# Kernel tuning notes

Hardware: AMD Instinct MI355X
Metric: run time of the kernel (lower is better)

The kernel has to match this reference:

```python
import jax, jax.numpy as jnp
import numpy as np

SEQ, BATCH, HID, NLAYERS = 2048, 16, 1024, 2


def setup_inputs() -> dict:
    key = jax.random.key(0)
    ks = jax.random.split(key, 3)
    scale = 1.0 / np.sqrt(HID)
    x = jax.random.normal(ks[0], (SEQ, BATCH, HID), dtype=jnp.float32)
    W0 = jax.random.normal(ks[1], (HID, 3 * HID), dtype=jnp.float32) * scale
    b0 = jnp.zeros((2 * HID,), dtype=jnp.float32)
    W1 = jax.random.normal(ks[2], (HID, 3 * HID), dtype=jnp.float32) * scale
    b1 = jnp.zeros((2 * HID,), dtype=jnp.float32)
    return {"x": x, "W0": W0, "b0": b0, "W1": W1, "b1": b1}


def _sru_layer(x, W, b):
    # x: [L, B, H]; W: [H, 3H]; b: [2H]
    L, B, H = x.shape
    U = jnp.einsum('lbd,dk->lbk', x, W)  # [L, B, 3H]
    x_tilde = U[..., :H]
    bf, br = b[:H], b[H:]
    f = jax.nn.sigmoid(U[..., H:2 * H] + bf)  # forget gate [L,B,H]
    r = jax.nn.sigmoid(U[..., 2 * H:] + br)   # reset gate  [L,B,H]

    def step(c_prev, inp):
        xt_t, f_t = inp
        c_t = f_t * c_prev + (1.0 - f_t) * xt_t
        return c_t, c_t

    c0 = jnp.zeros((B, H), dtype=x.dtype)
    _, cs = jax.lax.scan(step, c0, (x_tilde, f))  # cs: [L, B, H]
    h = r * cs + (1.0 - r) * x  # highway connection
    return h


def reference(x, W0, b0, W1, b1):
    h = _sru_layer(x, W0, b0)
    h = _sru_layer(h, W1, b1)
    return h[-1:]  # [1, B, H], matching `out[-1:]`
```

## Files before the change

kernel.cpp:

```cpp
#include <hip/hip_runtime.h>

#define SEQ    2048
#define BATCH  16
#define HID    1024
#define M_TOT  (SEQ*BATCH)
#define NCH    (BATCH*HID)
#define NCHUNK 64
#define TCHUNK (SEQ/NCHUNK)
#define NSEG   128

typedef __attribute__((ext_vector_type(8))) short          short8;
typedef __attribute__((ext_vector_type(8))) unsigned short ushort8_t;
typedef __attribute__((ext_vector_type(4))) float          floatx4;

__device__ __forceinline__ unsigned short f32_to_bf16(float f) {
  unsigned int u = __float_as_uint(f);
  u += 0x7FFFu + ((u >> 16) & 1u);
  return (unsigned short)(u >> 16);
}
__device__ __forceinline__ float bf16_to_f32(unsigned short h) {
  return __uint_as_float(((unsigned int)h) << 16);
}
__device__ __forceinline__ float sigmoidf_(float x) {
  return 1.f / (1.f + __expf(-x));
}


__device__ __forceinline__ void cast_swizzle_body(const float* __restrict__ src,
    unsigned short* __restrict__ dst, int mt, int kt, int t) {
  __shared__ unsigned short tile[4096];
  const int r = t >> 1, kh = (t & 1) * 16;
  const float* sp = src + (size_t)(mt * 128 + r) * 1024 + kt * 32 + kh;
  float4 v0 = *(const float4*)(sp + 0);
  float4 v1 = *(const float4*)(sp + 4);
  float4 v2 = *(const float4*)(sp + 8);
  float4 v3 = *(const float4*)(sp + 12);
  ushort8_t u0, u1;
  u0[0]=f32_to_bf16(v0.x); u0[1]=f32_to_bf16(v0.y); u0[2]=f32_to_bf16(v0.z); u0[3]=f32_to_bf16(v0.w);
  u0[4]=f32_to_bf16(v1.x); u0[5]=f32_to_bf16(v1.y); u0[6]=f32_to_bf16(v1.z); u0[7]=f32_to_bf16(v1.w);
  u1[0]=f32_to_bf16(v2.x); u1[1]=f32_to_bf16(v2.y); u1[2]=f32_to_bf16(v2.z); u1[3]=f32_to_bf16(v2.w);
  u1[4]=f32_to_bf16(v3.x); u1[5]=f32_to_bf16(v3.y); u1[6]=f32_to_bf16(v3.z); u1[7]=f32_to_bf16(v3.w);
  const int c = r >> 4, lr = r & 15, q0 = kh >> 3;
  const int unit0 = c * 64 + (q0 << 4) + lr;
  *(ushort8_t*)&tile[unit0 * 8]        = u0;
  *(ushort8_t*)&tile[(unit0 + 16) * 8] = u1;
  __syncthreads();
  const size_t base = ((size_t)mt * 32 + kt) * 4096;
  *(ushort8_t*)&dst[base + t * 16]     = *(const ushort8_t*)&tile[t * 16];
  *(ushort8_t*)&dst[base + t * 16 + 8] = *(const ushort8_t*)&tile[t * 16 + 8];
}

__device__ __forceinline__ void w_prep_body(const float* __restrict__ W,
    unsigned short* __restrict__ Wsw, int nt, int kt, int t) {
  __shared__ unsigned short tile[4096];
  const int kk = t >> 3, n0 = (t & 7) * 16;
  const float* sp = W + (size_t)(kt * 32 + kk) * 3072 + nt * 128 + n0;
  float v[16];
#pragma unroll
  for (int i = 0; i < 16; i += 4) {
    float4 f = *(const float4*)(sp + i);
    v[i] = f.x; v[i+1] = f.y; v[i+2] = f.z; v[i+3] = f.w;
  }
  const int cbase = (n0 >> 4) * 64 + ((kk >> 3) << 4);
#pragma unroll
  for (int j = 0; j < 16; j++)
    tile[(cbase + j) * 8 + (kk & 7)] = f32_to_bf16(v[j]);
  __syncthreads();
  const size_t base = ((size_t)nt * 32 + kt) * 4096;
  *(ushort8_t*)&Wsw[base + t * 16]     = *(const ushort8_t*)&tile[t * 16];
  *(ushort8_t*)&Wsw[base + t * 16 + 8] = *(const ushort8_t*)&tile[t * 16 + 8];
}

__global__ __launch_bounds__(256) void prep_all(const float* __restrict__ x,
    const float* __restrict__ W0, const float* __restrict__ W1,
    unsigned short* __restrict__ xsw, unsigned short* __restrict__ W0sw,
    unsigned short* __restrict__ W1sw) {
  const int id = blockIdx.x, t = threadIdx.x;
  if (id < 8192)        cast_swizzle_body(x, xsw, id >> 5, id & 31, t);
  else if (id < 8960)   w_prep_body(W0, W0sw, (id - 8192) >> 5, (id - 8192) & 31, t);
  else                  w_prep_body(W1, W1sw, (id - 8960) >> 5, (id - 8960) & 31, t);
}

typedef __attribute__((address_space(1))) const unsigned int GUI;
typedef __attribute__((address_space(3))) unsigned int LUI;
__device__ __forceinline__ void gl16(const unsigned short* g, unsigned short* l) {
  __builtin_amdgcn_global_load_lds((GUI*)g, (LUI*)l, 16, 0, 0);
}
__device__ __forceinline__ void barrier_fence() {
  asm volatile("s_barrier" ::: "memory");
}

__global__ __launch_bounds__(512, 2) void gemm_pipe(
    const unsigned short* __restrict__ A, const unsigned short* __restrict__ B,
    unsigned short* __restrict__ Xt, unsigned short* __restrict__ Fo,
    unsigned short* __restrict__ Ro, const float* __restrict__ bias)
{
  __shared__ unsigned short lds[65536];
  const int tid = threadIdx.x;
  const int wave = tid >> 6, lane = tid & 63;
  const int wm = wave >> 2, wn = wave & 3;
  const int id = blockIdx.x;
  const int xcd = id & 7, slot = id >> 3;
  const int g = slot / 96, r = slot % 96;
  const int bn = r >> 3;
  const int bm = xcd * 16 + g * 8 + (r & 7);

  const unsigned short* aSrc0 = A + ((size_t)(2 * bm + 0) * 32) * 4096 + tid * 8;
  const unsigned short* aSrc1 = A + ((size_t)(2 * bm + 1) * 32) * 4096 + tid * 8;
  const unsigned short* bSrc0 = B + ((size_t)(2 * bn + 0) * 32) * 4096 + tid * 8;
  const unsigned short* bSrc1 = B + ((size_t)(2 * bn + 1) * 32) * 4096 + tid * 8;

  floatx4 acc[8][4];
#pragma unroll
  for (int i = 0; i < 8; i++)
#pragma unroll
    for (int j = 0; j < 4; j++)
#pragma unroll
      for (int rr = 0; rr < 4; rr++) acc[i][j][rr] = 0.f;

#pragma unroll
  for (int u = 0; u < 3; ++u) {
    unsigned short* d = &lds[u * 16384 + wave * 512];
    gl16(aSrc0 + (size_t)u * 4096, d);
    gl16(aSrc1 + (size_t)u * 4096, d + 4096);
    gl16(bSrc0 + (size_t)u * 4096, d + 8192);
    gl16(bSrc1 + (size_t)u * 4096, d + 12288);
  }
  asm volatile("s_waitcnt vmcnt(0)" ::: "memory");
  barrier_fence();

  const int aoff = wm * 4096 + lane * 8;
  const int boff = 8192 + (wn >> 1) * 4096 + (wn & 1) * 2048 + lane * 8;

#pragma unroll 1
  for (int t = 0; t < 32; ++t) {
    const int sb = (t & 3) * 16384;
    const int u = t + 3;
    const unsigned short* As = &lds[sb + aoff];
    const unsigned short* Bs = &lds[sb + boff];
    short8 br[4], ar[4];
#pragma unroll
    for (int nj = 0; nj < 4; ++nj) br[nj] = *(const short8*)(Bs + nj * 512);
#pragma unroll
    for (int mi = 0; mi < 4; ++mi) ar[mi] = *(const short8*)(As + mi * 512);
    if (u < 32) {
      unsigned short* d = &lds[(u & 3) * 16384 + wave * 512];
      gl16(aSrc0 + (size_t)u * 4096, d);
      gl16(aSrc1 + (size_t)u * 4096, d + 4096);
    }
    __builtin_amdgcn_s_setprio(1);
#pragma unroll
    for (int mi = 0; mi < 4; ++mi)
#pragma unroll
      for (int nj = 0; nj < 4; ++nj)
        acc[mi][nj] = __builtin_amdgcn_mfma_f32_16x16x32_bf16(ar[mi], br[nj], acc[mi][nj], 0, 0, 0);
    __builtin_amdgcn_s_setprio(0);
#pragma unroll
    for (int mi = 0; mi < 4; ++mi) ar[mi] = *(const short8*)(As + (4 + mi) * 512);
    if (u < 32) {
      unsigned short* d = &lds[(u & 3) * 16384 + wave * 512];
      gl16(bSrc0 + (size_t)u * 4096, d + 8192);
      gl16(bSrc1 + (size_t)u * 4096, d + 12288);
    }
    __builtin_amdgcn_s_setprio(1);
#pragma unroll
    for (int mi = 0; mi < 4; ++mi)
#pragma unroll
      for (int nj = 0; nj < 4; ++nj)
        acc[4 + mi][nj] = __builtin_amdgcn_mfma_f32_16x16x32_bf16(ar[mi], br[nj], acc[4 + mi][nj], 0, 0, 0);
    __builtin_amdgcn_s_setprio(0);
    if (t <= 28)      asm volatile("s_waitcnt vmcnt(8)" ::: "memory");
    else if (t == 29) asm volatile("s_waitcnt vmcnt(4)" ::: "memory");
    else if (t == 30) asm volatile("s_waitcnt vmcnt(0)" ::: "memory");
    barrier_fence();
  }

  const int region = bn >> 2;
  const int cc = lane & 15, q = lane >> 4;
  const int lc0 = (bn & 3) * 256 + wn * 64 + cc;
  const int row0 = bm * 256 + wm * 128 + q * 4;
  if (region == 0) {
#pragma unroll
    for (int mi = 0; mi < 8; ++mi)
#pragma unroll
      for (int rg = 0; rg < 4; ++rg)
#pragma unroll
        for (int nj = 0; nj < 4; ++nj)
          Xt[(size_t)(row0 + mi * 16 + rg) * 1024 + lc0 + nj * 16] =
              f32_to_bf16(acc[mi][nj][rg]);
  } else {
    unsigned short* O = (region == 1) ? Fo : Ro;
    const float* bp = bias + (region - 1) * 1024;
    float bb[4];
#pragma unroll
    for (int nj = 0; nj < 4; ++nj) bb[nj] = bp[lc0 + nj * 16];
#pragma unroll
    for (int mi = 0; mi < 8; ++mi)
#pragma unroll
      for (int rg = 0; rg < 4; ++rg)
#pragma unroll
        for (int nj = 0; nj < 4; ++nj) {
          float s = sigmoidf_(acc[mi][nj][rg] + bb[nj]);
          O[(size_t)(row0 + mi * 16 + rg) * 1024 + lc0 + nj * 16] = f32_to_bf16(s);
        }
  }
}

__global__ __launch_bounds__(512, 2) void gemm2_scan(
    const unsigned short* __restrict__ A, const unsigned short* __restrict__ B,
    const float* __restrict__ bias, float* __restrict__ Pseg, float* __restrict__ Sseg)
{
  __shared__ unsigned short lds[65536];
  const int tid = threadIdx.x;
  const int wave = tid >> 6, lane = tid & 63;
  const int wm = wave >> 2, wn = wave & 3;
  const int id = blockIdx.x;
  const int xcd = id & 7, slot = id >> 3;
  const int bn = slot >> 4;
  const int bm = xcd * 16 + (slot & 15);

  const unsigned short* aSrc0 = A + ((size_t)(2 * bm + 0) * 32) * 4096 + tid * 8;
  const unsigned short* aSrc1 = A + ((size_t)(2 * bm + 1) * 32) * 4096 + tid * 8;
  const unsigned short* bxSrc = B + ((size_t)bn * 32) * 4096 + tid * 8;
  const unsigned short* bfSrc = B + ((size_t)(8 + bn) * 32) * 4096 + tid * 8;

  floatx4 ax[8][2], af[8][2];
#pragma unroll
  for (int i = 0; i < 8; i++)
#pragma unroll
    for (int j = 0; j < 2; j++)
#pragma unroll
      for (int rr = 0; rr < 4; rr++) { ax[i][j][rr] = 0.f; af[i][j][rr] = 0.f; }

#pragma unroll
  for (int u = 0; u < 3; ++u) {
    unsigned short* d = &lds[u * 16384 + wave * 512];
    gl16(aSrc0 + (size_t)u * 4096, d);
    gl16(aSrc1 + (size_t)u * 4096, d + 4096);
    gl16(bxSrc + (size_t)u * 4096, d + 8192);
    gl16(bfSrc + (size_t)u * 4096, d + 12288);
  }
  asm volatile("s_waitcnt vmcnt(0)" ::: "memory");
  barrier_fence();

  const int aoff  = wm * 4096 + lane * 8;
  const int bxoff = 8192  + wn * 1024 + lane * 8;
  const int bfoff = 12288 + wn * 1024 + lane * 8;

#pragma unroll 1
  for (int t = 0; t < 32; ++t) {
    const int sb = (t & 3) * 16384;
    const int u = t + 3;
    const unsigned short* As  = &lds[sb + aoff];
    const unsigned short* Bxs = &lds[sb + bxoff];
    const unsigned short* Bfs = &lds[sb + bfoff];
    short8 bx[2], bf[2], ar[4];
#pragma unroll
    for (int nj = 0; nj < 2; ++nj) {
      bx[nj] = *(const short8*)(Bxs + nj * 512);
      bf[nj] = *(const short8*)(Bfs + nj * 512);
    }
#pragma unroll
    for (int mi = 0; mi < 4; ++mi) ar[mi] = *(const short8*)(As + mi * 512);
    if (u < 32) {
      unsigned short* d = &lds[(u & 3) * 16384 + wave * 512];
      gl16(aSrc0 + (size_t)u * 4096, d);
      gl16(aSrc1 + (size_t)u * 4096, d + 4096);
    }
    __builtin_amdgcn_s_setprio(1);
#pragma unroll
    for (int mi = 0; mi < 4; ++mi)
#pragma unroll
      for (int nj = 0; nj < 2; ++nj) {
        ax[mi][nj] = __builtin_amdgcn_mfma_f32_16x16x32_bf16(ar[mi], bx[nj], ax[mi][nj], 0, 0, 0);
        af[mi][nj] = __builtin_amdgcn_mfma_f32_16x16x32_bf16(ar[mi], bf[nj], af[mi][nj], 0, 0, 0);
      }
    __builtin_amdgcn_s_setprio(0);
#pragma unroll
    for (int mi = 0; mi < 4; ++mi) ar[mi] = *(const short8*)(As + (4 + mi) * 512);
    if (u < 32) {
      unsigned short* d = &lds[(u & 3) * 16384 + wave * 512];
      gl16(bxSrc + (size_t)u * 4096, d + 8192);
      gl16(bfSrc + (size_t)u * 4096, d + 12288);
    }
    __builtin_amdgcn_s_setprio(1);
#pragma unroll
    for (int mi = 0; mi < 4; ++mi)
#pragma unroll
      for (int nj = 0; nj < 2; ++nj) {
        ax[4 + mi][nj] = __builtin_amdgcn_mfma_f32_16x16x32_bf16(ar[mi], bx[nj], ax[4 + mi][nj], 0, 0, 0);
        af[4 + mi][nj] = __builtin_amdgcn_mfma_f32_16x16x32_bf16(ar[mi], bf[nj], af[4 + mi][nj], 0, 0, 0);
      }
    __builtin_amdgcn_s_setprio(0);
    if (t <= 28)      asm volatile("s_waitcnt vmcnt(8)" ::: "memory");
    else if (t == 29) asm volatile("s_waitcnt vmcnt(4)" ::: "memory");
    else if (t == 30) asm volatile("s_waitcnt vmcnt(0)" ::: "memory");
    barrier_fence();
  }

  const int q = lane >> 4, cc = lane & 15;
  float pv[2][4], sv[2][4];
#pragma unroll
  for (int nj = 0; nj < 2; ++nj) {
    float bb = bias[bn * 128 + wn * 32 + nj * 16 + cc];
#pragma unroll
    for (int rg = 0; rg < 4; ++rg) {
      float p = 1.f, s = 0.f;
#pragma unroll
      for (int mi = 0; mi < 8; ++mi) {
        float f  = sigmoidf_(af[mi][nj][rg] + bb);
        float xt = ax[mi][nj][rg];
        s = f * s + (1.f - f) * xt;
        p *= f;
      }
      pv[nj][rg] = p; sv[nj][rg] = s;
    }
  }
  float* lf = (float*)lds;
  __syncthreads();
  if (wm == 0) {
#pragma unroll
    for (int nj = 0; nj < 2; ++nj)
#pragma unroll
      for (int rg = 0; rg < 4; ++rg) {
        const int idx = (((wn * 64 + lane) * 4 + rg) * 2 + nj) * 2;
        lf[idx]     = pv[nj][rg];
        lf[idx + 1] = sv[nj][rg];
      }
  }
  __syncthreads();
  if (wm == 1) {
#pragma unroll
    for (int nj = 0; nj < 2; ++nj) {
      const int h = bn * 128 + wn * 32 + nj * 16 + cc;
#pragma unroll
      for (int rg = 0; rg < 4; ++rg) {
        const int idx = (((wn * 64 + lane) * 4 + rg) * 2 + nj) * 2;
        float plo = lf[idx], slo = lf[idx + 1];
        float phi = pv[nj][rg], shi = sv[nj][rg];
        const size_t off = (size_t)bm * NCH + (q * 4 + rg) * 1024 + h;
        Pseg[off] = plo * phi;
        Sseg[off] = phi * slo + shi;
      }
    }
  }
}

__global__ __launch_bounds__(256) void scan_pass1(
    const unsigned short* __restrict__ Xt, const unsigned short* __restrict__ F,
    float* __restrict__ P, float* __restrict__ S) {
  const int ch = (blockIdx.x * 256 + threadIdx.x) * 8;
  const int chunk = blockIdx.y;
  size_t idx = (size_t)chunk * TCHUNK * NCH + ch;
  float p[8], s[8];
#pragma unroll
  for (int j = 0; j < 8; j++) { p[j] = 1.f; s[j] = 0.f; }
  for (int t = 0; t < TCHUNK; ++t) {
    ushort8_t fv = *(const ushort8_t*)&F[idx];
    ushort8_t xv = *(const ushort8_t*)&Xt[idx];
#pragma unroll
    for (int j = 0; j < 8; j++) {
      float f  = bf16_to_f32(fv[j]);
      float xt = bf16_to_f32(xv[j]);
      s[j] = f * s[j] + (1.f - f) * xt;
      p[j] *= f;
    }
    idx += NCH;
  }
  float4* P4 = (float4*)&P[(size_t)chunk * NCH + ch];
  float4* S4 = (float4*)&S[(size_t)chunk * NCH + ch];
  P4[0] = make_float4(p[0], p[1], p[2], p[3]);
  P4[1] = make_float4(p[4], p[5], p[6], p[7]);
  S4[0] = make_float4(s[0], s[1], s[2], s[3]);
  S4[1] = make_float4(s[4], s[5], s[6], s[7]);
}

__global__ __launch_bounds__(256) void combine_c0(
    const float* __restrict__ P, const float* __restrict__ S, float* __restrict__ C0) {
  const int ch = blockIdx.x * 256 + threadIdx.x;
  float c = 0.f;
#pragma unroll 4
  for (int k = 0; k < NCHUNK; ++k) {
    C0[(size_t)k * NCH + ch] = c;
    c = P[(size_t)k * NCH + ch] * c + S[(size_t)k * NCH + ch];
  }
}

#define TPAD 4112
__global__ __launch_bounds__(256) void scan1_pass2_fused(
    const unsigned short* __restrict__ Xt, const unsigned short* __restrict__ F,
    const unsigned short* __restrict__ R, unsigned short* __restrict__ xsw,
    const float* __restrict__ C0, unsigned short* __restrict__ h1last)
{
  __shared__ unsigned short st[4 * TPAD];
  const int hb = blockIdx.x;
  const int chunk = blockIdx.y;
  const int tid = threadIdx.x;
  const int b = tid >> 4, hg = tid & 15;
  const int h0 = hb * 128 + hg * 8;
  const int ch = b * 1024 + h0;
  const int tl   = hg >> 2;
  const int usub = (hg & 3) * 16 + b;

  float c[8];
  {
    const float4* C4 = (const float4*)&C0[(size_t)chunk * NCH + ch];
    float4 a = C4[0], d = C4[1];
    c[0]=a.x; c[1]=a.y; c[2]=a.z; c[3]=a.w; c[4]=d.x; c[5]=d.y; c[6]=d.z; c[7]=d.w;
  }

  size_t idx = (size_t)chunk * TCHUNK * NCH + ch;
  for (int t8 = 0; t8 < TCHUNK / 8; ++t8) {
#pragma unroll
    for (int ts = 0; ts < 8; ++ts) {
      const int t = chunk * TCHUNK + t8 * 8 + ts;
      ushort8_t fv = *(const ushort8_t*)&F[idx];
      ushort8_t xv = *(const ushort8_t*)&Xt[idx];
      ushort8_t rv = *(const ushort8_t*)&R[idx];
      const size_t soff = ((size_t)(t >> 3) * 32 + (h0 >> 5)) * 4096
                        + (size_t)(((t & 7) * 64 + usub) * 8);
      ushort8_t xo = *(const ushort8_t*)&xsw[soff];
      ushort8_t hv;
#pragma unroll
      for (int j = 0; j < 8; ++j) {
        float f  = bf16_to_f32(fv[j]);
        float xt = bf16_to_f32(xv[j]);
        c[j] = f * c[j] + (1.f - f) * xt;
        float r  = bf16_to_f32(rv[j]);
        float xval = bf16_to_f32(xo[j]);
        hv[j] = f32_to_bf16(r * c[j] + (1.f - r) * xval);
      }
      *(ushort8_t*)&st[tl * TPAD + (ts * 64 + usub) * 8] = hv;
      if (t == SEQ - 1) *(ushort8_t*)&h1last[ch] = hv;
      idx += NCH;
    }
    __syncthreads();
    const size_t gbase = (((size_t)chunk * (TCHUNK / 8) + t8) * 32 + hb * 4) * 4096;
#pragma unroll
    for (int tl2 = 0; tl2 < 4; ++tl2) {
      size_t gdst = gbase + (size_t)tl2 * 4096 + tid * 16;
      *(ushort8_t*)&xsw[gdst]     = *(const ushort8_t*)&st[tl2 * TPAD + tid * 16];
      *(ushort8_t*)&xsw[gdst + 8] = *(const ushort8_t*)&st[tl2 * TPAD + tid * 16 + 8];
    }
    __syncthreads();
  }
}

__global__ __launch_bounds__(256) void r2_kernel(
    const unsigned short* __restrict__ h1last, const float* __restrict__ W1,
    const float* __restrict__ b1, float* __restrict__ r2) {
  __shared__ float xrow[1024];
  const int b = blockIdx.x, nq = blockIdx.y, tid = threadIdx.x;
  for (int i = tid; i < 1024; i += 256)
    xrow[i] = bf16_to_f32(h1last[b * 1024 + i]);
  __syncthreads();
  const int n = nq * 256 + tid;
  float acc = b1[1024 + n];
  for (int d = 0; d < 1024; ++d)
    acc += xrow[d] * W1[(size_t)d * 3072 + 2048 + n];
  r2[b * 1024 + n] = sigmoidf_(acc);
}

__global__ __launch_bounds__(256) void final_l2(
    const float* __restrict__ Pseg, const float* __restrict__ Sseg,
    const float* __restrict__ r2, const unsigned short* __restrict__ h1last,
    float* __restrict__ out) {
  const int ch = blockIdx.x * 256 + threadIdx.x;
  float c = 0.f;
#pragma unroll 8
  for (int k = 0; k < NSEG; ++k)
    c = Pseg[(size_t)k * NCH + ch] * c + Sseg[(size_t)k * NCH + ch];
  float r = r2[ch];
  float x = bf16_to_f32(h1last[ch]);
  out[ch] = r * c + (1.f - r) * x;
}

extern "C" void kernel_launch(void* const* d_in, const int* in_sizes, int n_in,
                              void* d_out, int out_size, void* d_ws, size_t ws_size,
                              hipStream_t stream) {
  const float* x  = (const float*)d_in[0];
  const float* W0 = (const float*)d_in[1];
  const float* b0 = (const float*)d_in[2];
  const float* W1 = (const float*)d_in[3];
  const float* b1 = (const float*)d_in[4];
  float* out = (float*)d_out;

  char* ws = (char*)d_ws;
  auto alloc = [&](size_t bytes) {
    char* p = ws; ws += (bytes + 255) & ~(size_t)255; return p;
  };
  const size_t NE = (size_t)M_TOT * HID;
  unsigned short* xsw   = (unsigned short*)alloc(NE * 2);
  unsigned short* W0sw  = (unsigned short*)alloc((size_t)3072 * 1024 * 2);
  unsigned short* W1sw  = (unsigned short*)alloc((size_t)3072 * 1024 * 2);
  unsigned short* Xt    = (unsigned short*)alloc(NE * 2);
  unsigned short* F     = (unsigned short*)alloc(NE * 2);
  unsigned short* R     = (unsigned short*)alloc(NE * 2);
  unsigned short* h1last= (unsigned short*)alloc((size_t)NCH * 2);
  float* P    = (float*)alloc((size_t)NCHUNK * NCH * 4);
  float* S    = (float*)alloc((size_t)NCHUNK * NCH * 4);
  float* C0   = (float*)alloc((size_t)NCHUNK * NCH * 4);
  float* Pseg = (float*)alloc((size_t)NSEG * NCH * 4);
  float* Sseg = (float*)alloc((size_t)NSEG * NCH * 4);
  float* r2   = (float*)alloc((size_t)NCH * 4);

  dim3 blk256(256);
  prep_all<<<dim3(9728), blk256, 0, stream>>>(x, W0, W1, xsw, W0sw, W1sw);
  gemm_pipe<<<dim3(1536), dim3(512), 0, stream>>>(xsw, W0sw, Xt, F, R, b0);
  scan_pass1<<<dim3(8, NCHUNK), blk256, 0, stream>>>(Xt, F, P, S);
  combine_c0<<<dim3(NCH / 256), blk256, 0, stream>>>(P, S, C0);
  scan1_pass2_fused<<<dim3(8, NCHUNK), blk256, 0, stream>>>(Xt, F, R, xsw, C0, h1last);
  r2_kernel<<<dim3(16, 4), blk256, 0, stream>>>(h1last, W1, b1, r2);
  gemm2_scan<<<dim3(1024), dim3(512), 0, stream>>>(xsw, W1sw, b1, Pseg, Sseg);
  final_l2<<<dim3(NCH / 256), blk256, 0, stream>>>(Pseg, Sseg, r2, h1last, out);
}
```

Baseline: 731.6 us.

## Fuse layer-1 scan pass1 into GEMM epilogue with 8-step segments

Layer-1 GEMM now tiles so each block computes matching x~, f and r columns for 128 rows, which is 8 timesteps of 16 batch. The epilogue computes per-segment scan products and sums directly from the accumulators and writes Pseg1/Sseg1, so the separate scan_pass1 kernel and its re-read of Xt/F are gone. The scan pass2 now runs over 256 segments of 8 steps, and combine_c0 walks 256 segments instead of 64. In exchange the GEMM tile shape changes to 128x(3x128), which uses a smaller per-operand tile and may cost GEMM efficiency, and the P/S/C0 buffers grow.

```diff
diff --git a/kernel.cpp b/kernel.cpp
--- a/kernel.cpp
+++ b/kernel.cpp
@@ -5,8 +5,7 @@
 #define HID    1024
 #define M_TOT  (SEQ*BATCH)
 #define NCH    (BATCH*HID)
-#define NCHUNK 64
-#define TCHUNK (SEQ/NCHUNK)
+#define NSEG1  256
 #define NSEG   128
 
 typedef __attribute__((ext_vector_type(8))) short          short8;
@@ -90,10 +89,11 @@
   asm volatile("s_barrier" ::: "memory");
 }
 
-__global__ __launch_bounds__(512, 2) void gemm_pipe(
+__global__ __launch_bounds__(512, 2) void gemm1_scan(
     const unsigned short* __restrict__ A, const unsigned short* __restrict__ B,
     unsigned short* __restrict__ Xt, unsigned short* __restrict__ Fo,
-    unsigned short* __restrict__ Ro, const float* __restrict__ bias)
+    unsigned short* __restrict__ Ro, const float* __restrict__ bias,
+    float* __restrict__ Pseg1, float* __restrict__ Sseg1)
 {
   __shared__ unsigned short lds[65536];
   const int tid = threadIdx.x;
@@ -101,73 +101,81 @@
   const int wm = wave >> 2, wn = wave & 3;
   const int id = blockIdx.x;
   const int xcd = id & 7, slot = id >> 3;
-  const int g = slot / 96, r = slot % 96;
-  const int bn = r >> 3;
-  const int bm = xcd * 16 + g * 8 + (r & 7);
-
-  const unsigned short* aSrc0 = A + ((size_t)(2 * bm + 0) * 32) * 4096 + tid * 8;
-  const unsigned short* aSrc1 = A + ((size_t)(2 * bm + 1) * 32) * 4096 + tid * 8;
-  const unsigned short* bSrc0 = B + ((size_t)(2 * bn + 0) * 32) * 4096 + tid * 8;
-  const unsigned short* bSrc1 = B + ((size_t)(2 * bn + 1) * 32) * 4096 + tid * 8;
-
-  floatx4 acc[8][4];
-#pragma unroll
-  for (int i = 0; i < 8; i++)
-#pragma unroll
-    for (int j = 0; j < 4; j++)
-#pragma unroll
-      for (int rr = 0; rr < 4; rr++) acc[i][j][rr] = 0.f;
+  const int bn = slot >> 5;
+  const int bm = xcd * 32 + (slot & 31);
+
+  const unsigned short* aSrc  = A + ((size_t)bm * 32) * 4096 + tid * 8;
+  const unsigned short* bxSrc = B + ((size_t)bn * 32) * 4096 + tid * 8;
+  const unsigned short* bfSrc = B + ((size_t)(8 + bn) * 32) * 4096 + tid * 8;
+  const unsigned short* brSrc = B + ((size_t)(16 + bn) * 32) * 4096 + tid * 8;
+
+  floatx4 ax[4][2], af[4][2], arr[4][2];
+#pragma unroll
+  for (int i = 0; i < 4; i++)
+#pragma unroll
+    for (int j = 0; j < 2; j++)
+#pragma unroll
+      for (int rr = 0; rr < 4; rr++) { ax[i][j][rr] = 0.f; af[i][j][rr] = 0.f; arr[i][j][rr] = 0.f; }
 
 #pragma unroll
   for (int u = 0; u < 3; ++u) {
     unsigned short* d = &lds[u * 16384 + wave * 512];
-    gl16(aSrc0 + (size_t)u * 4096, d);
-    gl16(aSrc1 + (size_t)u * 4096, d + 4096);
-    gl16(bSrc0 + (size_t)u * 4096, d + 8192);
-    gl16(bSrc1 + (size_t)u * 4096, d + 12288);
+    gl16(aSrc  + (size_t)u * 4096, d);
+    gl16(bxSrc + (size_t)u * 4096, d + 4096);
+    gl16(bfSrc + (size_t)u * 4096, d + 8192);
+    gl16(brSrc + (size_t)u * 4096, d + 12288);
   }
   asm volatile("s_waitcnt vmcnt(0)" ::: "memory");
   barrier_fence();
 
-  const int aoff = wm * 4096 + lane * 8;
-  const int boff = 8192 + (wn >> 1) * 4096 + (wn & 1) * 2048 + lane * 8;
+  const int aoff = wm * 2048 + lane * 8;
+  const int bxo  = 4096  + wn * 1024 + lane * 8;
+  const int bfo  = 8192  + wn * 1024 + lane * 8;
+  const int bro  = 12288 + wn * 1024 + lane * 8;
 
 #pragma unroll 1
   for (int t = 0; t < 32; ++t) {
     const int sb = (t & 3) * 16384;
     const int u = t + 3;
-    const unsigned short* As = &lds[sb + aoff];
-    const unsigned short* Bs = &lds[sb + boff];
-    short8 br[4], ar[4];
-#pragma unroll
-    for (int nj = 0; nj < 4; ++nj) br[nj] = *(const short8*)(Bs + nj * 512);
+    const unsigned short* As  = &lds[sb + aoff];
+    const unsigned short* Bxs = &lds[sb + bxo];
+    const unsigned short* Bfs = &lds[sb + bfo];
+    const unsigned short* Brs = &lds[sb + bro];
+    short8 ar[4], bx[2], bf[2], br2[2];
+#pragma unroll
+    for (int nj = 0; nj < 2; ++nj) {
+      bx[nj] = *(const short8*)(Bxs + nj * 512);
+      bf[nj] = *(const short8*)(Bfs + nj * 512);
+    }
 #pragma unroll
     for (int mi = 0; mi < 4; ++mi) ar[mi] = *(const short8*)(As + mi * 512);
     if (u < 32) {
       unsigned short* d = &lds[(u & 3) * 16384 + wave * 512];
-      gl16(aSrc0 + (size_t)u * 4096, d);
-      gl16(aSrc1 + (size_t)u * 4096, d + 4096);
+      gl16(aSrc  + (size_t)u * 4096, d);
+      gl16(bxSrc + (size_t)u * 4096, d + 4096);
     }
     __builtin_amdgcn_s_setprio(1);
 #pragma unroll
     for (int mi = 0; mi < 4; ++mi)
 #pragma unroll
-      for (int nj = 0; nj < 4; ++nj)
-        acc[mi][nj] = __builtin_amdgcn_mfma_f32_16x16x32_bf16(ar[mi], br[nj], acc[mi][nj], 0, 0, 0);
+      for (int nj = 0; nj < 2; ++nj) {
+        ax[mi][nj] = __builtin_amdgcn_mfma_f32_16x16x32_bf16(ar[mi], bx[nj], ax[mi][nj], 0, 0, 0);
+        af[mi][nj] = __builtin_amdgcn_mfma_f32_16x16x32_bf16(ar[mi], bf[nj], af[mi][nj], 0, 0, 0);
+      }
     __builtin_amdgcn_s_setprio(0);
 #pragma unroll
-    for (int mi = 0; mi < 4; ++mi) ar[mi] = *(const short8*)(As + (4 + mi) * 512);
+    for (int nj = 0; nj < 2; ++nj) br2[nj] = *(const short8*)(Brs + nj * 512);
     if (u < 32) {
       unsigned short* d = &lds[(u & 3) * 16384 + wave * 512];
-      gl16(bSrc0 + (size_t)u * 4096, d + 8192);
-      gl16(bSrc1 + (size_t)u * 4096, d + 12288);
+      gl16(bfSrc + (size_t)u * 4096, d + 8192);
+      gl16(brSrc + (size_t)u * 4096, d + 12288);
     }
     __builtin_amdgcn_s_setprio(1);
 #pragma unroll
     for (int mi = 0; mi < 4; ++mi)
 #pragma unroll
-      for (int nj = 0; nj < 4; ++nj)
-        acc[4 + mi][nj] = __builtin_amdgcn_mfma_f32_16x16x32_bf16(ar[mi], br[nj], acc[4 + mi][nj], 0, 0, 0);
+      for (int nj = 0; nj < 2; ++nj)
+        arr[mi][nj] = __builtin_amdgcn_mfma_f32_16x16x32_bf16(ar[mi], br2[nj], arr[mi][nj], 0, 0, 0);
     __builtin_amdgcn_s_setprio(0);
     if (t <= 28)      asm volatile("s_waitcnt vmcnt(8)" ::: "memory");
     else if (t == 29) asm volatile("s_waitcnt vmcnt(4)" ::: "memory");
@@ -175,34 +183,60 @@
     barrier_fence();
   }
 
-  const int region = bn >> 2;
-  const int cc = lane & 15, q = lane >> 4;
-  const int lc0 = (bn & 3) * 256 + wn * 64 + cc;
-  const int row0 = bm * 256 + wm * 128 + q * 4;
-  if (region == 0) {
-#pragma unroll
-    for (int mi = 0; mi < 8; ++mi)
-#pragma unroll
-      for (int rg = 0; rg < 4; ++rg)
-#pragma unroll
-        for (int nj = 0; nj < 4; ++nj)
-          Xt[(size_t)(row0 + mi * 16 + rg) * 1024 + lc0 + nj * 16] =
-              f32_to_bf16(acc[mi][nj][rg]);
-  } else {
-    unsigned short* O = (region == 1) ? Fo : Ro;
-    const float* bp = bias + (region - 1) * 1024;
-    float bb[4];
-#pragma unroll
-    for (int nj = 0; nj < 4; ++nj) bb[nj] = bp[lc0 + nj * 16];
-#pragma unroll
-    for (int mi = 0; mi < 8; ++mi)
-#pragma unroll
-      for (int rg = 0; rg < 4; ++rg)
-#pragma unroll
-        for (int nj = 0; nj < 4; ++nj) {
-          float s = sigmoidf_(acc[mi][nj][rg] + bb[nj]);
-          O[(size_t)(row0 + mi * 16 + rg) * 1024 + lc0 + nj * 16] = f32_to_bf16(s);
-        }
+  const int q = lane >> 4, cc = lane & 15;
+  const int h0 = bn * 128 + wn * 32 + cc;
+  const int row0 = bm * 128 + wm * 64 + q * 4;
+  float bbf[2], bbr[2];
+#pragma unroll
+  for (int nj = 0; nj < 2; ++nj) {
+    bbf[nj] = bias[h0 + nj * 16];
+    bbr[nj] = bias[1024 + h0 + nj * 16];
+  }
+  float pv[2][4], sv[2][4];
+#pragma unroll
+  for (int nj = 0; nj < 2; ++nj)
+#pragma unroll
+    for (int rg = 0; rg < 4; ++rg) {
+      float p = 1.f, s = 0.f;
+#pragma unroll
+      for (int mi = 0; mi < 4; ++mi) {
+        float xt = ax[mi][nj][rg];
+        float f  = sigmoidf_(af[mi][nj][rg] + bbf[nj]);
+        float rr = sigmoidf_(arr[mi][nj][rg] + bbr[nj]);
+        const size_t ro = (size_t)(row0 + mi * 16 + rg) * 1024 + h0 + nj * 16;
+        Xt[ro] = f32_to_bf16(xt);
+        Fo[ro] = f32_to_bf16(f);
+        Ro[ro] = f32_to_bf16(rr);
+        s = f * s + (1.f - f) * xt;
+        p *= f;
+      }
+      pv[nj][rg] = p; sv[nj][rg] = s;
+    }
+  float* lf = (float*)lds;
+  __syncthreads();
+  if (wm == 0) {
+#pragma unroll
+    for (int nj = 0; nj < 2; ++nj)
+#pragma unroll
+      for (int rg = 0; rg < 4; ++rg) {
+        const int idx = (((wn * 64 + lane) * 4 + rg) * 2 + nj) * 2;
+        lf[idx]     = pv[nj][rg];
+        lf[idx + 1] = sv[nj][rg];
+      }
+  }
+  __syncthreads();
+  if (wm == 1) {
+#pragma unroll
+    for (int nj = 0; nj < 2; ++nj)
+#pragma unroll
+      for (int rg = 0; rg < 4; ++rg) {
+        const int idx = (((wn * 64 + lane) * 4 + rg) * 2 + nj) * 2;
+        float plo = lf[idx], slo = lf[idx + 1];
+        float phi = pv[nj][rg], shi = sv[nj][rg];
+        const size_t off = (size_t)bm * NCH + (q * 4 + rg) * 1024 + h0 + nj * 16;
+        Pseg1[off] = plo * phi;
+        Sseg1[off] = phi * slo + shi;
+      }
   }
 }
 
@@ -346,41 +380,12 @@
   }
 }
 
-__global__ __launch_bounds__(256) void scan_pass1(
-    const unsigned short* __restrict__ Xt, const unsigned short* __restrict__ F,
-    float* __restrict__ P, float* __restrict__ S) {
-  const int ch = (blockIdx.x * 256 + threadIdx.x) * 8;
-  const int chunk = blockIdx.y;
-  size_t idx = (size_t)chunk * TCHUNK * NCH + ch;
-  float p[8], s[8];
-#pragma unroll
-  for (int j = 0; j < 8; j++) { p[j] = 1.f; s[j] = 0.f; }
-  for (int t = 0; t < TCHUNK; ++t) {
-    ushort8_t fv = *(const ushort8_t*)&F[idx];
-    ushort8_t xv = *(const ushort8_t*)&Xt[idx];
-#pragma unroll
-    for (int j = 0; j < 8; j++) {
-      float f  = bf16_to_f32(fv[j]);
-      float xt = bf16_to_f32(xv[j]);
-      s[j] = f * s[j] + (1.f - f) * xt;
-      p[j] *= f;
-    }
-    idx += NCH;
-  }
-  float4* P4 = (float4*)&P[(size_t)chunk * NCH + ch];
-  float4* S4 = (float4*)&S[(size_t)chunk * NCH + ch];
-  P4[0] = make_float4(p[0], p[1], p[2], p[3]);
-  P4[1] = make_float4(p[4], p[5], p[6], p[7]);
-  S4[0] = make_float4(s[0], s[1], s[2], s[3]);
-  S4[1] = make_float4(s[4], s[5], s[6], s[7]);
-}
-
 __global__ __launch_bounds__(256) void combine_c0(
     const float* __restrict__ P, const float* __restrict__ S, float* __restrict__ C0) {
   const int ch = blockIdx.x * 256 + threadIdx.x;
   float c = 0.f;
-#pragma unroll 4
-  for (int k = 0; k < NCHUNK; ++k) {
+#pragma unroll 8
+  for (int k = 0; k < NSEG1; ++k) {
     C0[(size_t)k * NCH + ch] = c;
     c = P[(size_t)k * NCH + ch] * c + S[(size_t)k * NCH + ch];
   }
@@ -409,40 +414,37 @@
     c[0]=a.x; c[1]=a.y; c[2]=a.z; c[3]=a.w; c[4]=d.x; c[5]=d.y; c[6]=d.z; c[7]=d.w;
   }
 
-  size_t idx = (size_t)chunk * TCHUNK * NCH + ch;
-  for (int t8 = 0; t8 < TCHUNK / 8; ++t8) {
-#pragma unroll
-    for (int ts = 0; ts < 8; ++ts) {
-      const int t = chunk * TCHUNK + t8 * 8 + ts;
-      ushort8_t fv = *(const ushort8_t*)&F[idx];
-      ushort8_t xv = *(const ushort8_t*)&Xt[idx];
-      ushort8_t rv = *(const ushort8_t*)&R[idx];
-      const size_t soff = ((size_t)(t >> 3) * 32 + (h0 >> 5)) * 4096
-                        + (size_t)(((t & 7) * 64 + usub) * 8);
-      ushort8_t xo = *(const ushort8_t*)&xsw[soff];
-      ushort8_t hv;
-#pragma unroll
-      for (int j = 0; j < 8; ++j) {
-        float f  = bf16_to_f32(fv[j]);
-        float xt = bf16_to_f32(xv[j]);
-        c[j] = f * c[j] + (1.f - f) * xt;
-        float r  = bf16_to_f32(rv[j]);
-        float xval = bf16_to_f32(xo[j]);
-        hv[j] = f32_to_bf16(r * c[j] + (1.f - r) * xval);
-      }
-      *(ushort8_t*)&st[tl * TPAD + (ts * 64 + usub) * 8] = hv;
-      if (t == SEQ - 1) *(ushort8_t*)&h1last[ch] = hv;
-      idx += NCH;
-    }
-    __syncthreads();
-    const size_t gbase = (((size_t)chunk * (TCHUNK / 8) + t8) * 32 + hb * 4) * 4096;
-#pragma unroll
-    for (int tl2 = 0; tl2 < 4; ++tl2) {
-      size_t gdst = gbase + (size_t)tl2 * 4096 + tid * 16;
-      *(ushort8_t*)&xsw[gdst]     = *(const ushort8_t*)&st[tl2 * TPAD + tid * 16];
-      *(ushort8_t*)&xsw[gdst + 8] = *(const ushort8_t*)&st[tl2 * TPAD + tid * 16 + 8];
-    }
-    __syncthreads();
+  size_t idx = (size_t)chunk * 8 * NCH + ch;
+#pragma unroll
+  for (int ts = 0; ts < 8; ++ts) {
+    const int t = chunk * 8 + ts;
+    ushort8_t fv = *(const ushort8_t*)&F[idx];
+    ushort8_t xv = *(const ushort8_t*)&Xt[idx];
+    ushort8_t rv = *(const ushort8_t*)&R[idx];
+    const size_t soff = ((size_t)(t >> 3) * 32 + (h0 >> 5)) * 4096
+                      + (size_t)(((t & 7) * 64 + usub) * 8);
+    ushort8_t xo = *(const ushort8_t*)&xsw[soff];
+    ushort8_t hv;
+#pragma unroll
+    for (int j = 0; j < 8; ++j) {
+      float f  = bf16_to_f32(fv[j]);
+      float xt = bf16_to_f32(xv[j]);
+      c[j] = f * c[j] + (1.f - f) * xt;
+      float r  = bf16_to_f32(rv[j]);
+      float xval = bf16_to_f32(xo[j]);
+      hv[j] = f32_to_bf16(r * c[j] + (1.f - r) * xval);
+    }
+    *(ushort8_t*)&st[tl * TPAD + (ts * 64 + usub) * 8] = hv;
+    if (t == SEQ - 1) *(ushort8_t*)&h1last[ch] = hv;
+    idx += NCH;
+  }
+  __syncthreads();
+  const size_t gbase = ((size_t)chunk * 32 + hb * 4) * 4096;
+#pragma unroll
+  for (int tl2 = 0; tl2 < 4; ++tl2) {
+    size_t gdst = gbase + (size_t)tl2 * 4096 + tid * 16;
+    *(ushort8_t*)&xsw[gdst]     = *(const ushort8_t*)&st[tl2 * TPAD + tid * 16];
+    *(ushort8_t*)&xsw[gdst + 8] = *(const ushort8_t*)&st[tl2 * TPAD + tid * 16 + 8];
   }
 }
 
@@ -497,19 +499,18 @@
   unsigned short* F     = (unsigned short*)alloc(NE * 2);
   unsigned short* R     = (unsigned short*)alloc(NE * 2);
   unsigned short* h1last= (unsigned short*)alloc((size_t)NCH * 2);
-  float* P    = (float*)alloc((size_t)NCHUNK * NCH * 4);
-  float* S    = (float*)alloc((size_t)NCHUNK * NCH * 4);
-  float* C0   = (float*)alloc((size_t)NCHUNK * NCH * 4);
-  float* Pseg = (float*)alloc((size_t)NSEG * NCH * 4);
-  float* Sseg = (float*)alloc((size_t)NSEG * NCH * 4);
-  float* r2   = (float*)alloc((size_t)NCH * 4);
+  float* Pseg1 = (float*)alloc((size_t)NSEG1 * NCH * 4);
+  float* Sseg1 = (float*)alloc((size_t)NSEG1 * NCH * 4);
+  float* C0    = (float*)alloc((size_t)NSEG1 * NCH * 4);
+  float* Pseg  = (float*)alloc((size_t)NSEG * NCH * 4);
+  float* Sseg  = (float*)alloc((size_t)NSEG * NCH * 4);
+  float* r2    = (float*)alloc((size_t)NCH * 4);
 
   dim3 blk256(256);
   prep_all<<<dim3(9728), blk256, 0, stream>>>(x, W0, W1, xsw, W0sw, W1sw);
-  gemm_pipe<<<dim3(1536), dim3(512), 0, stream>>>(xsw, W0sw, Xt, F, R, b0);
-  scan_pass1<<<dim3(8, NCHUNK), blk256, 0, stream>>>(Xt, F, P, S);
-  combine_c0<<<dim3(NCH / 256), blk256, 0, stream>>>(P, S, C0);
-  scan1_pass2_fused<<<dim3(8, NCHUNK), blk256, 0, stream>>>(Xt, F, R, xsw, C0, h1last);
+  gemm1_scan<<<dim3(2048), dim3(512), 0, stream>>>(xsw, W0sw, Xt, F, R, b0, Pseg1, Sseg1);
+  combine_c0<<<dim3(NCH / 256), blk256, 0, stream>>>(Pseg1, Sseg1, C0);
+  scan1_pass2_fused<<<dim3(8, NSEG1), blk256, 0, stream>>>(Xt, F, R, xsw, C0, h1last);
   r2_kernel<<<dim3(16, 4), blk256, 0, stream>>>(h1last, W1, b1, r2);
   gemm2_scan<<<dim3(1024), dim3(512), 0, stream>>>(xsw, W1sw, b1, Pseg, Sseg);
   final_l2<<<dim3(NCH / 256), blk256, 0, stream>>>(Pseg, Sseg, r2, h1last, out);
```

Measured after the change: 776.2 us. 6.1% more time.
